# Kernel tuning notes

Measured on AMD Instinct MI355X. Metric: run time of the kernel, lower is better.

The kernel has to match this reference:

```python
import jax, jax.numpy as jnp
import numpy as np

N_NODES = 100000
N_EDGES = 3200000
IN_CH = 128
HID = 128
N_GRAPHS = 128
BN_EPS = 1e-5


def _gcn_conv(x, W, b, src, dst, n_nodes):
    # x: [N, Cin] -> [N, Cout]; PyG GCNConv: linear, add self-loops,
    # symmetric D^-1/2 A D^-1/2 normalization, scatter-add at dst, + bias.
    xw = x @ W  # [N, Cout]
    loop = jnp.arange(n_nodes, dtype=src.dtype)
    s = jnp.concatenate([src, loop])
    d = jnp.concatenate([dst, loop])
    deg = jax.ops.segment_sum(jnp.ones_like(d, dtype=xw.dtype), d, num_segments=n_nodes)
    dinv = jnp.where(deg > 0, jax.lax.rsqrt(deg), 0.0)
    coef = (dinv[s] * dinv[d])[:, None]  # [E+N, 1]
    msg = xw[s] * coef  # gather + scale
    out = jax.ops.segment_sum(msg, d, num_segments=n_nodes)  # scatter-add
    return out + b


def setup_inputs() -> dict:
    key = jax.random.key(0)
    ks = jax.random.split(key, 8)
    x = jax.random.normal(ks[0], (N_NODES, IN_CH), dtype=jnp.float32)
    edge_index = jax.random.randint(ks[1], (2, N_EDGES), 0, N_NODES, dtype=jnp.int64)
    batch = jnp.sort(jax.random.randint(ks[2], (N_NODES,), 0, N_GRAPHS, dtype=jnp.int64))
    W1 = jax.random.normal(ks[3], (IN_CH, HID), dtype=jnp.float32) / np.sqrt(IN_CH)
    W2 = jax.random.normal(ks[4], (HID, HID), dtype=jnp.float32) / np.sqrt(HID)
    fw1 = jax.random.normal(ks[5], (HID, HID // 2), dtype=jnp.float32) / np.sqrt(HID)
    cw = jax.random.normal(ks[6], (HID // 2, 2), dtype=jnp.float32) / np.sqrt(HID // 2)
    return {
        "x": x,
        "edge_index": edge_index,
        "batch": batch,
        "W1": W1,
        "b1": jnp.zeros((HID,), jnp.float32),
        "gamma": jnp.ones((HID,), jnp.float32),
        "beta": jnp.zeros((HID,), jnp.float32),
        "rmean": jnp.zeros((HID,), jnp.float32),
        "rvar": jnp.ones((HID,), jnp.float32),
        "W2": W2,
        "b2": jnp.zeros((HID,), jnp.float32),
        "fw1": fw1,
        "fb1": jnp.zeros((HID // 2,), jnp.float32),
        "cw": cw,
        "cb": jnp.zeros((2,), jnp.float32),
    }


def reference(x, edge_index, batch, W1, b1, gamma, beta, rmean, rvar, W2, b2, fw1, fb1, cw, cb):
    src, dst = edge_index[0], edge_index[1]
    h = _gcn_conv(x, W1, b1, src, dst, N_NODES)
    # BatchNorm1d in inference mode (running stats); dropout is identity in eval.
    h = (h - rmean) * jax.lax.rsqrt(rvar + BN_EPS) * gamma + beta
    h = jax.nn.relu(h)
    h = _gcn_conv(h, W2, b2, src, dst, N_NODES)
    # global_mean_pool over graphs
    sums = jax.ops.segment_sum(h, batch, num_segments=N_GRAPHS)  # [G, H]
    cnts = jax.ops.segment_sum(jnp.ones((N_NODES,), h.dtype), batch, num_segments=N_GRAPHS)
    pooled = sums / jnp.maximum(cnts, 1.0)[:, None]
    z = jax.nn.relu(pooled @ fw1 + fb1)
    return z @ cw + cb
```

## Files before the change

### kernel.cpp

```cpp
#include <hip/hip_runtime.h>
#include <hip/hip_bf16.h>

#define N_NODES 100000
#define N_EDGES 3200000
#define CH 128
#define NG 128
#define BN_EPS 1e-5f
#define NBUCK 1024
#define EPB 16384
#define NSPB 1563

using i32x4 = __attribute__((ext_vector_type(4))) int;

__device__ __forceinline__ unsigned int packq(const float* v, float inv) {
    int q0 = __float2int_rn(v[0] * inv), q1 = __float2int_rn(v[1] * inv);
    int q2 = __float2int_rn(v[2] * inv), q3 = __float2int_rn(v[3] * inv);
    return (unsigned int)(q0 & 255) | ((unsigned int)(q1 & 255) << 8) |
           ((unsigned int)(q2 & 255) << 16) | ((unsigned int)(q3 & 255) << 24);
}

__global__ __launch_bounds__(256) void k_quantx(const float* __restrict__ x,
                                                unsigned char* __restrict__ Xq,
                                                float* __restrict__ xs) {
    int t = threadIdx.x;
    int row = blockIdx.x * 16 + (t >> 4);
    int seg = t & 15;
    const float4* p = (const float4*)&x[(size_t)row * CH + seg * 8];
    float4 a = p[0], b = p[1];
    float v[8] = {a.x, a.y, a.z, a.w, b.x, b.y, b.z, b.w};
    float m = 0.f;
    #pragma unroll
    for (int i = 0; i < 8; ++i) m = fmaxf(m, fabsf(v[i]));
    m = fmaxf(m, __shfl_xor(m, 1, 64));
    m = fmaxf(m, __shfl_xor(m, 2, 64));
    m = fmaxf(m, __shfl_xor(m, 4, 64));
    m = fmaxf(m, __shfl_xor(m, 8, 64));
    float inv = (m > 0.f) ? 127.0f / m : 0.f;
    uint2 pk;
    pk.x = packq(&v[0], inv);
    pk.y = packq(&v[4], inv);
    *(uint2*)&Xq[(size_t)row * CH + seg * 8] = pk;
    if (seg == 0) xs[row] = m * (1.0f / 127.0f);
}

__global__ __launch_bounds__(256) void k_prepW(
    const float* __restrict__ W1, const float* __restrict__ W2,
    const float* __restrict__ gamma, const float* __restrict__ beta,
    const float* __restrict__ rmean, const float* __restrict__ rvar, const float* __restrict__ b1,
    unsigned char* __restrict__ Wq1T, float* __restrict__ wcs1,
    unsigned char* __restrict__ Wq2T, float* __restrict__ wcs2,
    float* __restrict__ A1, float* __restrict__ B1) {
    int t = threadIdx.x;
    const float* W = (t < 128) ? W1 : W2;
    unsigned char* WT = (t < 128) ? Wq1T : Wq2T;
    float* wcs = (t < 128) ? wcs1 : wcs2;
    int c = t & 127;
    float m = 0.f;
    for (int k = 0; k < 128; ++k) m = fmaxf(m, fabsf(W[k * CH + c]));
    float inv = (m > 0.f) ? 127.0f / m : 0.f;
    for (int k = 0; k < 128; ++k) {
        int q = __float2int_rn(W[k * CH + c] * inv);
        WT[c * CH + k] = (unsigned char)(q & 255);
    }
    wcs[c] = m * (1.0f / 127.0f);
    if (t < 128) {
        float a = gamma[c] * rsqrtf(rvar[c] + BN_EPS);
        A1[c] = a;
        B1[c] = (b1[c] - rmean[c]) * a + beta[c];
    }
}

__global__ __launch_bounds__(256) void k_bhist(const int* __restrict__ dst, int* __restrict__ bcnt) {
    __shared__ int lh[NBUCK];
    for (int i = threadIdx.x; i < NBUCK; i += 256) lh[i] = 0;
    __syncthreads();
    for (int e = blockIdx.x * 256 + threadIdx.x; e < N_EDGES; e += gridDim.x * 256)
        atomicAdd(&lh[dst[e] >> 7], 1);
    __syncthreads();
    for (int i = threadIdx.x; i < NBUCK; i += 256) {
        int v = lh[i];
        if (v) atomicAdd(&bcnt[i], v);
    }
}

__global__ __launch_bounds__(256) void k_bscan(const int* __restrict__ in, int* __restrict__ out,
                                               int* __restrict__ cur) {
    __shared__ int sm[256];
    int t = threadIdx.x;
    int4 v = *(const int4*)&in[t * 4];
    int tsum = v.x + v.y + v.z + v.w;
    sm[t] = tsum;
    __syncthreads();
    for (int off = 1; off < 256; off <<= 1) {
        int val = sm[t];
        int add = (t >= off) ? sm[t - off] : 0;
        __syncthreads();
        sm[t] = val + add;
        __syncthreads();
    }
    int excl = sm[t] - tsum;
    int o0 = excl, o1 = excl + v.x, o2 = o1 + v.y, o3 = o2 + v.z;
    out[t * 4] = o0; out[t * 4 + 1] = o1; out[t * 4 + 2] = o2; out[t * 4 + 3] = o3;
    if (cur) { cur[t * 4] = o0; cur[t * 4 + 1] = o1; cur[t * 4 + 2] = o2; cur[t * 4 + 3] = o3; }
}

__global__ __launch_bounds__(256) void k_bin(const int* __restrict__ src, const int* __restrict__ dst,
                                             int* __restrict__ bcur, unsigned int* __restrict__ pairs) {
    __shared__ int lhist[NBUCK];
    __shared__ int lbase[NBUCK];
    int t = threadIdx.x;
    for (int i = t; i < NBUCK; i += 256) lhist[i] = 0;
    __syncthreads();
    int base = blockIdx.x * EPB;
    int lim = min(base + EPB, N_EDGES);
    for (int e = base + t; e < lim; e += 256)
        atomicAdd(&lhist[dst[e] >> 7], 1);
    __syncthreads();
    for (int i = t; i < NBUCK; i += 256) {
        int h = lhist[i];
        lbase[i] = h ? atomicAdd(&bcur[i], h) : 0;
        lhist[i] = 0;
    }
    __syncthreads();
    for (int e = base + t; e < lim; e += 256) {
        int d = dst[e];
        int b = d >> 7;
        int r = atomicAdd(&lhist[b], 1);
        pairs[lbase[b] + r] = ((unsigned int)src[e] << 7) | ((unsigned int)d & 127u);
    }
}

__global__ __launch_bounds__(256) void k_bfill(const unsigned int* __restrict__ pairs,
                                               const int* __restrict__ boffs,
                                               int* __restrict__ offs, int* __restrict__ deg,
                                               float* __restrict__ dinv, int* __restrict__ perm) {
    __shared__ int lcur[1024];
    __shared__ int loff[1024];
    __shared__ int sm[256];
    int b = blockIdx.x;
    int t = threadIdx.x;
    for (int i = t; i < 1024; i += 256) lcur[i] = 0;
    __syncthreads();
    int p0 = boffs[b];
    int p1 = (b == NBUCK - 1) ? N_EDGES : boffs[b + 1];
    for (int p = p0 + t; p < p1; p += 256) {
        unsigned int e = pairs[p];
        int idx = (int)((e & 127u) << 3) | (int)((e >> 7) >> 14);
        atomicAdd(&lcur[idx], 1);
    }
    __syncthreads();
    int4 v = *(const int4*)&lcur[t * 4];
    int tsum = v.x + v.y + v.z + v.w;
    sm[t] = tsum;
    __syncthreads();
    for (int off = 1; off < 256; off <<= 1) {
        int val = sm[t];
        int add = (t >= off) ? sm[t - off] : 0;
        __syncthreads();
        sm[t] = val + add;
        __syncthreads();
    }
    int excl = sm[t] - tsum + p0;
    loff[t * 4]     = excl;
    loff[t * 4 + 1] = excl + v.x;
    loff[t * 4 + 2] = excl + v.x + v.y;
    loff[t * 4 + 3] = excl + v.x + v.y + v.z;
    lcur[t * 4] = 0; lcur[t * 4 + 1] = 0; lcur[t * 4 + 2] = 0; lcur[t * 4 + 3] = 0;
    __syncthreads();
    if (t < 128) {
        int node = (b << 7) + t;
        if (node < N_NODES) {
            int o0 = loff[t * 8];
            int o1 = (t == 127) ? p1 : loff[(t + 1) * 8];
            int cnt = o1 - o0;
            offs[node] = o0;
            deg[node] = cnt;
            dinv[node] = rsqrtf((float)(cnt + 1));
        }
    }
    __syncthreads();
    for (int p = p0 + t; p < p1; p += 256) {
        unsigned int e = pairs[p];
        int src = (int)(e >> 7);
        int idx = (int)((e & 127u) << 3) | (src >> 14);
        int r = atomicAdd(&lcur[idx], 1);
        perm[loff[idx] + r] = src;
    }
}

__global__ __launch_bounds__(256) void k_gemm_mfma(
    const unsigned char* __restrict__ Xq, const float* __restrict__ xs,
    const unsigned char* __restrict__ WT, const float* __restrict__ wcs,
    const float* __restrict__ dinvp, unsigned char* __restrict__ Yq, float* __restrict__ ospre) {
    __shared__ float ep[4][16][132];
    int t = threadIdx.x;
    int w = t >> 6;
    int lane = t & 63;
    int quad = lane >> 4, l16 = lane & 15;
    int row0 = blockIdx.x * 64 + w * 16;

    int arow = row0 + l16;
    if (arow >= N_NODES) arow = N_NODES - 1;
    i32x4 a0 = *(const i32x4*)&Xq[(size_t)arow * CH + quad * 16];
    i32x4 a1 = *(const i32x4*)&Xq[(size_t)arow * CH + 64 + quad * 16];

    i32x4 acc[8];
    #pragma unroll
    for (int i = 0; i < 8; ++i) acc[i] = (i32x4){0, 0, 0, 0};

    #pragma unroll
    for (int tt = 0; tt < 8; ++tt) {
        int n = tt * 16 + l16;
        i32x4 b0 = *(const i32x4*)&WT[(size_t)n * CH + quad * 16];
        i32x4 b1 = *(const i32x4*)&WT[(size_t)n * CH + 64 + quad * 16];
        acc[tt] = __builtin_amdgcn_mfma_i32_16x16x64_i8(a0, b0, acc[tt], 0, 0, 0);
        acc[tt] = __builtin_amdgcn_mfma_i32_16x16x64_i8(a1, b1, acc[tt], 0, 0, 0);
    }

    float xsr[4];
    #pragma unroll
    for (int r = 0; r < 4; ++r) {
        int rr = row0 + quad * 4 + r;
        xsr[r] = xs[(rr < N_NODES) ? rr : (N_NODES - 1)];
    }
    #pragma unroll
    for (int tt = 0; tt < 8; ++tt) {
        float wc = wcs[tt * 16 + l16];
        #pragma unroll
        for (int r = 0; r < 4; ++r)
            ep[w][quad * 4 + r][tt * 16 + l16] = (float)acc[tt][r] * xsr[r] * wc;
    }
    __syncthreads();

    int rl = lane >> 2, part = lane & 3;
    int grow = row0 + rl;
    float v[32];
    float m = 0.f;
    #pragma unroll
    for (int i = 0; i < 32; ++i) {
        v[i] = ep[w][rl][part * 32 + i];
        m = fmaxf(m, fabsf(v[i]));
    }
    m = fmaxf(m, __shfl_xor(m, 1, 64));
    m = fmaxf(m, __shfl_xor(m, 2, 64));
    if (grow < N_NODES) {
        float inv = (m > 0.f) ? 127.0f / m : 0.f;
        unsigned int o[8];
        #pragma unroll
        for (int q = 0; q < 8; ++q) o[q] = packq(&v[q * 4], inv);
        uint4* dst0 = (uint4*)&Yq[(size_t)grow * CH + part * 32];
        dst0[0] = make_uint4(o[0], o[1], o[2], o[3]);
        dst0[1] = make_uint4(o[4], o[5], o[6], o[7]);
        if (part == 0) ospre[grow] = (m * (1.0f / 127.0f)) * dinvp[grow];
    }
}

#define ACCI8(f, v)                                                                    \
    { int _a = (int)v.x, _b = (int)v.y;                                                \
      acc[0] += f * (float)((_a << 24) >> 24);                                         \
      acc[1] += f * (float)((_a << 16) >> 24);                                         \
      acc[2] += f * (float)((_a << 8) >> 24);                                          \
      acc[3] += f * (float)(_a >> 24);                                                 \
      acc[4] += f * (float)((_b << 24) >> 24);                                         \
      acc[5] += f * (float)((_b << 16) >> 24);                                         \
      acc[6] += f * (float)((_b << 8) >> 24);                                          \
      acc[7] += f * (float)(_b >> 24); }

#define SPMM_ROW_GATHER()                                                              \
    float di = 0.f; int beg = 0, end = 0;                                              \
    if (valid) { di = dinv[row]; beg = offs[row]; end = beg + deg[row]; }              \
    float acc[8];                                                                      \
    _Pragma("unroll") for (int j = 0; j < 8; ++j) acc[j] = 0.f;                        \
    for (int cb = beg; cb < end; cb += 8) {                                            \
        int k0 = cb + g, k1 = cb + g + 4;                                              \
        int ka0 = (k0 < end) ? k0 : (end - 1);                                         \
        int ka1 = (k1 < end) ? k1 : (end - 1);                                         \
        int s0 = perm[ka0], s1 = perm[ka1];                                            \
        float f0 = (k0 < end) ? di : 0.f;                                              \
        float f1 = (k1 < end) ? di : 0.f;                                              \
        f0 *= spre[s0]; f1 *= spre[s1];                                                \
        uint2 v0 = xq[(size_t)s0 * 16 + c];                                            \
        uint2 v1 = xq[(size_t)s1 * 16 + c];                                            \
        ACCI8(f0, v0) ACCI8(f1, v1)                                                    \
    }                                                                                  \
    _Pragma("unroll") for (int j = 0; j < 8; ++j) {                                    \
        acc[j] += __shfl_xor(acc[j], 16, 64);                                          \
        acc[j] += __shfl_xor(acc[j], 32, 64);                                          \
    }

__global__ __launch_bounds__(256) void k_spmm_bn_relu(
    const uint2* __restrict__ xq, const int* __restrict__ perm, const int* __restrict__ offs,
    const int* __restrict__ deg, const float* __restrict__ dinv, const float* __restrict__ spre,
    const float* __restrict__ A1, const float* __restrict__ B1,
    uint2* __restrict__ outq, float* __restrict__ osraw) {
    int w = threadIdx.x >> 6;
    int lane = threadIdx.x & 63;
    int g = lane >> 4, c = lane & 15;
    int base = blockIdx.x * 64;
    for (int i = 0; i < 16; ++i) {
        int row = __builtin_amdgcn_readfirstlane(base + i * 4 + w);
        bool valid = row < N_NODES;
        SPMM_ROW_GATHER()
        if (g == 0 && valid) {
            uint2 v = xq[(size_t)row * 16 + c];
            float fs = di * spre[row];
            ACCI8(fs, v)
            int ch = c * 8;
            float r[8];
            const float4* A4 = (const float4*)&A1[ch];
            const float4* B4 = (const float4*)&B1[ch];
            #pragma unroll
            for (int q = 0; q < 2; ++q) {
                float4 aa = A4[q], bb = B4[q];
                r[q * 4 + 0] = fmaxf(acc[q * 4 + 0] * aa.x + bb.x, 0.f);
                r[q * 4 + 1] = fmaxf(acc[q * 4 + 1] * aa.y + bb.y, 0.f);
                r[q * 4 + 2] = fmaxf(acc[q * 4 + 2] * aa.z + bb.z, 0.f);
                r[q * 4 + 3] = fmaxf(acc[q * 4 + 3] * aa.w + bb.w, 0.f);
            }
            float m = 0.f;
            #pragma unroll
            for (int j = 0; j < 8; ++j) m = fmaxf(m, r[j]);
            #pragma unroll
            for (int off = 1; off < 16; off <<= 1) m = fmaxf(m, __shfl_xor(m, off, 64));
            float inv = (m > 0.f) ? 127.0f / m : 0.f;
            uint2 pk;
            pk.x = packq(&r[0], inv);
            pk.y = packq(&r[4], inv);
            outq[(size_t)row * 16 + c] = pk;
            if (c == 0) osraw[row] = m * (1.0f / 127.0f);
        }
    }
}

__global__ __launch_bounds__(256) void k_spmm_pool(
    const uint2* __restrict__ xq, const int* __restrict__ perm, const int* __restrict__ offs,
    const int* __restrict__ deg, const float* __restrict__ dinv, const float* __restrict__ spre,
    const float* __restrict__ bias, const int* __restrict__ batch,
    float* __restrict__ psum, int* __restrict__ pcnt) {
    __shared__ float red[4][128];
    __shared__ int gid[4];
    int w = threadIdx.x >> 6;
    int lane = threadIdx.x & 63;
    int g = lane >> 4, c = lane & 15;
    int base = blockIdx.x * 64;
    for (int i = 0; i < 16; ++i) {
        int row = __builtin_amdgcn_readfirstlane(base + i * 4 + w);
        bool valid = row < N_NODES;
        SPMM_ROW_GATHER()
        if (g == 0) {
            int ch = c * 8;
            if (valid) {
                uint2 v = xq[(size_t)row * 16 + c];
                float fs = di * spre[row];
                ACCI8(fs, v)
                #pragma unroll
                for (int j = 0; j < 8; ++j) red[w][ch + j] = acc[j] + bias[ch + j];
            } else {
                #pragma unroll
                for (int j = 0; j < 8; ++j) red[w][ch + j] = 0.f;
            }
        }
        if (lane == 0) gid[w] = valid ? batch[row] : -1;
        __syncthreads();
        bool same = (gid[0] >= 0) && (gid[0] == gid[1]) && (gid[1] == gid[2]) && (gid[2] == gid[3]);
        int c0 = lane * 2;
        if (same) {
            if (w == 0) {
                float sx = red[0][c0] + red[1][c0] + red[2][c0] + red[3][c0];
                float sy = red[0][c0 + 1] + red[1][c0 + 1] + red[2][c0 + 1] + red[3][c0 + 1];
                unsafeAtomicAdd(&psum[gid[0] * CH + c0], sx);
                unsafeAtomicAdd(&psum[gid[0] * CH + c0 + 1], sy);
                if (lane == 0) atomicAdd(&pcnt[gid[0]], 4);
            }
        } else if (gid[w] >= 0) {
            unsafeAtomicAdd(&psum[gid[w] * CH + c0], red[w][c0]);
            unsafeAtomicAdd(&psum[gid[w] * CH + c0 + 1], red[w][c0 + 1]);
            if (lane == 0) atomicAdd(&pcnt[gid[w]], 1);
        }
        __syncthreads();
    }
}

__global__ __launch_bounds__(128) void k_head(const float* __restrict__ psum, const int* __restrict__ pcnt,
                                              const float* __restrict__ fw1, const float* __restrict__ fb1,
                                              const float* __restrict__ cw, const float* __restrict__ cb,
                                              float* __restrict__ out) {
    __shared__ float fws[128 * 64];
    for (int i = threadIdx.x; i < 128 * 64; i += 128) fws[i] = fw1[i];
    __syncthreads();
    int g = threadIdx.x;
    float z[64];
    #pragma unroll
    for (int j = 0; j < 64; ++j) z[j] = fb1[j];
    float cnt = fmaxf((float)pcnt[g], 1.f);
    float inv = 1.f / cnt;
    for (int c = 0; c < 128; ++c) {
        float p = psum[g * CH + c] * inv;
        #pragma unroll
        for (int j = 0; j < 64; ++j) z[j] += p * fws[c * 64 + j];
    }
    float o0 = cb[0], o1 = cb[1];
    #pragma unroll
    for (int j = 0; j < 64; ++j) {
        float zz = fmaxf(z[j], 0.f);
        o0 += zz * cw[j * 2];
        o1 += zz * cw[j * 2 + 1];
    }
    out[g * 2] = o0;
    out[g * 2 + 1] = o1;
}

extern "C" void kernel_launch(void* const* d_in, const int* in_sizes, int n_in,
                              void* d_out, int out_size, void* d_ws, size_t ws_size,
                              hipStream_t stream) {
    const float* x     = (const float*)d_in[0];
    const int*   ei    = (const int*)d_in[1];
    const int*   batch = (const int*)d_in[2];
    const float* W1    = (const float*)d_in[3];
    const float* b1    = (const float*)d_in[4];
    const float* gamma = (const float*)d_in[5];
    const float* beta  = (const float*)d_in[6];
    const float* rmean = (const float*)d_in[7];
    const float* rvar  = (const float*)d_in[8];
    const float* W2    = (const float*)d_in[9];
    const float* b2    = (const float*)d_in[10];
    const float* fw1   = (const float*)d_in[11];
    const float* fb1   = (const float*)d_in[12];
    const float* cw    = (const float*)d_in[13];
    const float* cb    = (const float*)d_in[14];
    const int* srcp = ei;
    const int* dstp = ei + N_EDGES;

    char* w = (char*)d_ws;
    int*   bcnt  = (int*)w;   w += 4096;
    float* psum  = (float*)w; w += 65536;
    int*   pcnt  = (int*)w;   w += 512;
    size_t zbytes = 4096 + 65536 + 512;
    int*   deg   = (int*)w;   w += 400000;
    int*   offs  = (int*)w;   w += 400000;
    float* dinv  = (float*)w; w += 400000;
    float* xsA   = (float*)w; w += 400000;
    float* spreA = (float*)w; w += 400000;
    float* srawB = (float*)w; w += 400000;
    float* spreC = (float*)w; w += 400000;
    float* A1    = (float*)w; w += 512;
    float* B1    = (float*)w; w += 512;
    float* wcs1  = (float*)w; w += 512;
    float* wcs2  = (float*)w; w += 512;
    unsigned char* Wq1T = (unsigned char*)w; w += 16384;
    unsigned char* Wq2T = (unsigned char*)w; w += 16384;
    int*   boffs = (int*)w;   w += 4096;
    int*   bcur  = (int*)w;   w += 4096;
    unsigned int* pairs = (unsigned int*)w; w += 12800000;
    int*   perm  = (int*)w;   w += 12800000;
    unsigned char* Xq   = (unsigned char*)w; w += 12800000;
    unsigned char* bufA = (unsigned char*)w; w += 12800000;
    unsigned char* bufB = (unsigned char*)w; w += 12800000;
    unsigned char* bufC = (unsigned char*)w; w += 12800000;

    hipMemsetAsync(d_ws, 0, zbytes, stream);
    k_quantx<<<6250, 256, 0, stream>>>(x, Xq, xsA);
    k_bhist<<<200, 256, 0, stream>>>(dstp, bcnt);
    k_bscan<<<1, 256, 0, stream>>>(bcnt, boffs, bcur);
    k_bin<<<(N_EDGES + EPB - 1) / EPB, 256, 0, stream>>>(srcp, dstp, bcur, pairs);
    k_bfill<<<NBUCK, 256, 0, stream>>>(pairs, boffs, offs, deg, dinv, perm);
    k_prepW<<<1, 256, 0, stream>>>(W1, W2, gamma, beta, rmean, rvar, b1,
                                   Wq1T, wcs1, Wq2T, wcs2, A1, B1);
    k_gemm_mfma<<<1563, 256, 0, stream>>>(Xq, xsA, Wq1T, wcs1, dinv, bufA, spreA);
    k_spmm_bn_relu<<<NSPB, 256, 0, stream>>>((const uint2*)bufA, perm, offs, deg, dinv, spreA,
                                             A1, B1, (uint2*)bufB, srawB);
    k_gemm_mfma<<<1563, 256, 0, stream>>>(bufB, srawB, Wq2T, wcs2, dinv, bufC, spreC);
    k_spmm_pool<<<NSPB, 256, 0, stream>>>((const uint2*)bufC, perm, offs, deg, dinv, spreC,
                                          b2, batch, psum, pcnt);
    k_head<<<1, 128, 0, stream>>>(psum, pcnt, fw1, fb1, cw, cb, (float*)d_out);
}
```

Measured before the change: 555.3 us.

## Fuse input quantization into first GEMM and interleave two rows per SpMM wave

Drops the separate quantize-x kernel. The first GEMM now reads fp32 x directly, computes a per-row scale and packs int8 in registers before the MFMA, which saves a write and re-read of the quantized matrix and one launch. The SpMM kernels now gather two destination rows at once per wave, using 4 edges per step per row instead of 8 for one row. This gives more independent loads in flight, but lanes sit idle when the two rows have different degrees. The epilogues move into helper functions.

```diff
diff --git a/kernel.cpp b/kernel.cpp
--- a/kernel.cpp
+++ b/kernel.cpp
@@ -17,30 +17,6 @@
     int q2 = __float2int_rn(v[2] * inv), q3 = __float2int_rn(v[3] * inv);
     return (unsigned int)(q0 & 255) | ((unsigned int)(q1 & 255) << 8) |
            ((unsigned int)(q2 & 255) << 16) | ((unsigned int)(q3 & 255) << 24);
-}
-
-__global__ __launch_bounds__(256) void k_quantx(const float* __restrict__ x,
-                                                unsigned char* __restrict__ Xq,
-                                                float* __restrict__ xs) {
-    int t = threadIdx.x;
-    int row = blockIdx.x * 16 + (t >> 4);
-    int seg = t & 15;
-    const float4* p = (const float4*)&x[(size_t)row * CH + seg * 8];
-    float4 a = p[0], b = p[1];
-    float v[8] = {a.x, a.y, a.z, a.w, b.x, b.y, b.z, b.w};
-    float m = 0.f;
-    #pragma unroll
-    for (int i = 0; i < 8; ++i) m = fmaxf(m, fabsf(v[i]));
-    m = fmaxf(m, __shfl_xor(m, 1, 64));
-    m = fmaxf(m, __shfl_xor(m, 2, 64));
-    m = fmaxf(m, __shfl_xor(m, 4, 64));
-    m = fmaxf(m, __shfl_xor(m, 8, 64));
-    float inv = (m > 0.f) ? 127.0f / m : 0.f;
-    uint2 pk;
-    pk.x = packq(&v[0], inv);
-    pk.y = packq(&v[4], inv);
-    *(uint2*)&Xq[(size_t)row * CH + seg * 8] = pk;
-    if (seg == 0) xs[row] = m * (1.0f / 127.0f);
 }
 
 __global__ __launch_bounds__(256) void k_prepW(
@@ -188,6 +164,96 @@
     }
 }
 
+__global__ __launch_bounds__(256) void k_gemm_f32(
+    const float* __restrict__ X,
+    const unsigned char* __restrict__ WT, const float* __restrict__ wcs,
+    const float* __restrict__ dinvp, unsigned char* __restrict__ Yq, float* __restrict__ ospre) {
+    __shared__ float ep[4][16][132];
+    int t = threadIdx.x;
+    int w = t >> 6;
+    int lane = t & 63;
+    int quad = lane >> 4, l16 = lane & 15;
+    int row0 = blockIdx.x * 64 + w * 16;
+
+    int arow = row0 + l16;
+    if (arow >= N_NODES) arow = N_NODES - 1;
+
+    float xv[32];
+    {
+        const float4* p0 = (const float4*)&X[(size_t)arow * CH + quad * 16];
+        const float4* p1 = (const float4*)&X[(size_t)arow * CH + 64 + quad * 16];
+        #pragma unroll
+        for (int q = 0; q < 4; ++q) {
+            float4 f = p0[q];
+            xv[q * 4 + 0] = f.x; xv[q * 4 + 1] = f.y; xv[q * 4 + 2] = f.z; xv[q * 4 + 3] = f.w;
+        }
+        #pragma unroll
+        for (int q = 0; q < 4; ++q) {
+            float4 f = p1[q];
+            xv[16 + q * 4 + 0] = f.x; xv[16 + q * 4 + 1] = f.y;
+            xv[16 + q * 4 + 2] = f.z; xv[16 + q * 4 + 3] = f.w;
+        }
+    }
+    float m = 0.f;
+    #pragma unroll
+    for (int j = 0; j < 32; ++j) m = fmaxf(m, fabsf(xv[j]));
+    m = fmaxf(m, __shfl_xor(m, 16, 64));
+    m = fmaxf(m, __shfl_xor(m, 32, 64));
+    float inv = (m > 0.f) ? 127.0f / m : 0.f;
+    float ms = m * (1.0f / 127.0f);
+    unsigned int pk[8];
+    #pragma unroll
+    for (int j = 0; j < 8; ++j) pk[j] = packq(&xv[j * 4], inv);
+    i32x4 a0 = (i32x4){(int)pk[0], (int)pk[1], (int)pk[2], (int)pk[3]};
+    i32x4 a1 = (i32x4){(int)pk[4], (int)pk[5], (int)pk[6], (int)pk[7]};
+
+    i32x4 acc[8];
+    #pragma unroll
+    for (int i = 0; i < 8; ++i) acc[i] = (i32x4){0, 0, 0, 0};
+    #pragma unroll
+    for (int tt = 0; tt < 8; ++tt) {
+        int n = tt * 16 + l16;
+        i32x4 b0 = *(const i32x4*)&WT[(size_t)n * CH + quad * 16];
+        i32x4 b1 = *(const i32x4*)&WT[(size_t)n * CH + 64 + quad * 16];
+        acc[tt] = __builtin_amdgcn_mfma_i32_16x16x64_i8(a0, b0, acc[tt], 0, 0, 0);
+        acc[tt] = __builtin_amdgcn_mfma_i32_16x16x64_i8(a1, b1, acc[tt], 0, 0, 0);
+    }
+
+    float xsr[4];
+    #pragma unroll
+    for (int r = 0; r < 4; ++r) xsr[r] = __shfl(ms, quad * 4 + r, 64);
+    #pragma unroll
+    for (int tt = 0; tt < 8; ++tt) {
+        float wc = wcs[tt * 16 + l16];
+        #pragma unroll
+        for (int r = 0; r < 4; ++r)
+            ep[w][quad * 4 + r][tt * 16 + l16] = (float)acc[tt][r] * xsr[r] * wc;
+    }
+    __syncthreads();
+
+    int rl = lane >> 2, part = lane & 3;
+    int grow = row0 + rl;
+    float v[32];
+    float mm = 0.f;
+    #pragma unroll
+    for (int i = 0; i < 32; ++i) {
+        v[i] = ep[w][rl][part * 32 + i];
+        mm = fmaxf(mm, fabsf(v[i]));
+    }
+    mm = fmaxf(mm, __shfl_xor(mm, 1, 64));
+    mm = fmaxf(mm, __shfl_xor(mm, 2, 64));
+    if (grow < N_NODES) {
+        float inv2 = (mm > 0.f) ? 127.0f / mm : 0.f;
+        unsigned int o[8];
+        #pragma unroll
+        for (int q = 0; q < 8; ++q) o[q] = packq(&v[q * 4], inv2);
+        uint4* dst0 = (uint4*)&Yq[(size_t)grow * CH + part * 32];
+        dst0[0] = make_uint4(o[0], o[1], o[2], o[3]);
+        dst0[1] = make_uint4(o[4], o[5], o[6], o[7]);
+        if (part == 0) ospre[grow] = (mm * (1.0f / 127.0f)) * dinvp[grow];
+    }
+}
+
 __global__ __launch_bounds__(256) void k_gemm_mfma(
     const unsigned char* __restrict__ Xq, const float* __restrict__ xs,
     const unsigned char* __restrict__ WT, const float* __restrict__ wcs,
@@ -255,7 +321,7 @@
     }
 }
 
-#define ACCI8(f, v)                                                                    \
+#define ACCI8P(acc, f, v)                                                              \
     { int _a = (int)v.x, _b = (int)v.y;                                                \
       acc[0] += f * (float)((_a << 24) >> 24);                                         \
       acc[1] += f * (float)((_a << 16) >> 24);                                         \
@@ -266,27 +332,107 @@
       acc[6] += f * (float)((_b << 8) >> 24);                                          \
       acc[7] += f * (float)(_b >> 24); }
 
-#define SPMM_ROW_GATHER()                                                              \
-    float di = 0.f; int beg = 0, end = 0;                                              \
-    if (valid) { di = dinv[row]; beg = offs[row]; end = beg + deg[row]; }              \
-    float acc[8];                                                                      \
-    _Pragma("unroll") for (int j = 0; j < 8; ++j) acc[j] = 0.f;                        \
-    for (int cb = beg; cb < end; cb += 8) {                                            \
-        int k0 = cb + g, k1 = cb + g + 4;                                              \
-        int ka0 = (k0 < end) ? k0 : (end - 1);                                         \
-        int ka1 = (k1 < end) ? k1 : (end - 1);                                         \
-        int s0 = perm[ka0], s1 = perm[ka1];                                            \
-        float f0 = (k0 < end) ? di : 0.f;                                              \
-        float f1 = (k1 < end) ? di : 0.f;                                              \
-        f0 *= spre[s0]; f1 *= spre[s1];                                                \
-        uint2 v0 = xq[(size_t)s0 * 16 + c];                                            \
-        uint2 v1 = xq[(size_t)s1 * 16 + c];                                            \
-        ACCI8(f0, v0) ACCI8(f1, v1)                                                    \
+#define SPMM_PAIR_GATHER(ii)                                                           \
+    int rowA = __builtin_amdgcn_readfirstlane(base + (ii) * 4 + w);                    \
+    int rowB = __builtin_amdgcn_readfirstlane(base + (ii) * 4 + 4 + w);                \
+    bool valA = rowA < N_NODES, valB = rowB < N_NODES;                                 \
+    float diA = 0.f, diB = 0.f;                                                        \
+    int begA = 0, endA = 0, begB = 0, endB = 0;                                        \
+    if (valA) { diA = dinv[rowA]; begA = offs[rowA]; endA = begA + deg[rowA]; }        \
+    if (valB) { diB = dinv[rowB]; begB = offs[rowB]; endB = begB + deg[rowB]; }        \
+    float accA[8], accB[8];                                                            \
+    _Pragma("unroll") for (int j = 0; j < 8; ++j) { accA[j] = 0.f; accB[j] = 0.f; }    \
+    int cbA = begA, cbB = begB;                                                        \
+    while (cbA < endA || cbB < endB) {                                                 \
+        int kA = cbA + g, kB = cbB + g;                                                \
+        int kaA = (kA < endA) ? kA : ((endA > 1) ? endA - 1 : 0);                      \
+        int kaB = (kB < endB) ? kB : ((endB > 1) ? endB - 1 : 0);                      \
+        int sA = perm[kaA], sB = perm[kaB];                                            \
+        float fA = (kA < endA) ? diA : 0.f;                                            \
+        float fB = (kB < endB) ? diB : 0.f;                                            \
+        fA *= spre[sA]; fB *= spre[sB];                                                \
+        uint2 vA = xq[(size_t)sA * 16 + c];                                            \
+        uint2 vB = xq[(size_t)sB * 16 + c];                                            \
+        ACCI8P(accA, fA, vA) ACCI8P(accB, fB, vB)                                      \
+        cbA += 4; cbB += 4;                                                            \
     }                                                                                  \
     _Pragma("unroll") for (int j = 0; j < 8; ++j) {                                    \
-        acc[j] += __shfl_xor(acc[j], 16, 64);                                          \
-        acc[j] += __shfl_xor(acc[j], 32, 64);                                          \
-    }
+        accA[j] += __shfl_xor(accA[j], 16, 64);                                        \
+        accA[j] += __shfl_xor(accA[j], 32, 64);                                        \
+        accB[j] += __shfl_xor(accB[j], 16, 64);                                        \
+        accB[j] += __shfl_xor(accB[j], 32, 64);                                        \
+    }
+
+__device__ __forceinline__ void bn_epi(int row, float di, float* acc, int c,
+                                       const uint2* __restrict__ xq, const float* __restrict__ spre,
+                                       const float* __restrict__ A1, const float* __restrict__ B1,
+                                       uint2* __restrict__ outq, float* __restrict__ osraw) {
+    uint2 v = xq[(size_t)row * 16 + c];
+    float fs = di * spre[row];
+    ACCI8P(acc, fs, v)
+    int ch = c * 8;
+    float r[8];
+    const float4* A4 = (const float4*)&A1[ch];
+    const float4* B4 = (const float4*)&B1[ch];
+    #pragma unroll
+    for (int q = 0; q < 2; ++q) {
+        float4 aa = A4[q], bb = B4[q];
+        r[q * 4 + 0] = fmaxf(acc[q * 4 + 0] * aa.x + bb.x, 0.f);
+        r[q * 4 + 1] = fmaxf(acc[q * 4 + 1] * aa.y + bb.y, 0.f);
+        r[q * 4 + 2] = fmaxf(acc[q * 4 + 2] * aa.z + bb.z, 0.f);
+        r[q * 4 + 3] = fmaxf(acc[q * 4 + 3] * aa.w + bb.w, 0.f);
+    }
+    float m = 0.f;
+    #pragma unroll
+    for (int i = 0; i < 8; ++i) m = fmaxf(m, r[i]);
+    #pragma unroll
+    for (int off = 1; off < 16; off <<= 1) m = fmaxf(m, __shfl_xor(m, off, 64));
+    float inv = (m > 0.f) ? 127.0f / m : 0.f;
+    uint2 pk;
+    pk.x = packq(&r[0], inv);
+    pk.y = packq(&r[4], inv);
+    outq[(size_t)row * 16 + c] = pk;
+    if (c == 0) osraw[row] = m * (1.0f / 127.0f);
+}
+
+__device__ __forceinline__ void pool_epi(int row, bool valid, float di, float* acc,
+                                         int w, int lane, int g, int c,
+                                         const uint2* __restrict__ xq, const float* __restrict__ spre,
+                                         const float* __restrict__ bias, const int* __restrict__ batch,
+                                         float* __restrict__ psum, int* __restrict__ pcnt,
+                                         float (*red)[128], int* gid) {
+    if (g == 0) {
+        int ch = c * 8;
+        if (valid) {
+            uint2 v = xq[(size_t)row * 16 + c];
+            float fs = di * spre[row];
+            ACCI8P(acc, fs, v)
+            #pragma unroll
+            for (int j = 0; j < 8; ++j) red[w][ch + j] = acc[j] + bias[ch + j];
+        } else {
+            #pragma unroll
+            for (int j = 0; j < 8; ++j) red[w][ch + j] = 0.f;
+        }
+    }
+    if (lane == 0) gid[w] = valid ? batch[row] : -1;
+    __syncthreads();
+    bool same = (gid[0] >= 0) && (gid[0] == gid[1]) && (gid[1] == gid[2]) && (gid[2] == gid[3]);
+    int c0 = lane * 2;
+    if (same) {
+        if (w == 0) {
+            float sx = red[0][c0] + red[1][c0] + red[2][c0] + red[3][c0];
+            float sy = red[0][c0 + 1] + red[1][c0 + 1] + red[2][c0 + 1] + red[3][c0 + 1];
+            unsafeAtomicAdd(&psum[gid[0] * CH + c0], sx);
+            unsafeAtomicAdd(&psum[gid[0] * CH + c0 + 1], sy);
+            if (lane == 0) atomicAdd(&pcnt[gid[0]], 4);
+        }
+    } else if (gid[w] >= 0) {
+        unsafeAtomicAdd(&psum[gid[w] * CH + c0], red[w][c0]);
+        unsafeAtomicAdd(&psum[gid[w] * CH + c0 + 1], red[w][c0 + 1]);
+        if (lane == 0) atomicAdd(&pcnt[gid[w]], 1);
+    }
+    __syncthreads();
+}
 
 __global__ __launch_bounds__(256) void k_spmm_bn_relu(
     const uint2* __restrict__ xq, const int* __restrict__ perm, const int* __restrict__ offs,
@@ -297,38 +443,10 @@
     int lane = threadIdx.x & 63;
     int g = lane >> 4, c = lane & 15;
     int base = blockIdx.x * 64;
-    for (int i = 0; i < 16; ++i) {
-        int row = __builtin_amdgcn_readfirstlane(base + i * 4 + w);
-        bool valid = row < N_NODES;
-        SPMM_ROW_GATHER()
-        if (g == 0 && valid) {
-            uint2 v = xq[(size_t)row * 16 + c];
-            float fs = di * spre[row];
-            ACCI8(fs, v)
-            int ch = c * 8;
-            float r[8];
-            const float4* A4 = (const float4*)&A1[ch];
-            const float4* B4 = (const float4*)&B1[ch];
-            #pragma unroll
-            for (int q = 0; q < 2; ++q) {
-                float4 aa = A4[q], bb = B4[q];
-                r[q * 4 + 0] = fmaxf(acc[q * 4 + 0] * aa.x + bb.x, 0.f);
-                r[q * 4 + 1] = fmaxf(acc[q * 4 + 1] * aa.y + bb.y, 0.f);
-                r[q * 4 + 2] = fmaxf(acc[q * 4 + 2] * aa.z + bb.z, 0.f);
-                r[q * 4 + 3] = fmaxf(acc[q * 4 + 3] * aa.w + bb.w, 0.f);
-            }
-            float m = 0.f;
-            #pragma unroll
-            for (int j = 0; j < 8; ++j) m = fmaxf(m, r[j]);
-            #pragma unroll
-            for (int off = 1; off < 16; off <<= 1) m = fmaxf(m, __shfl_xor(m, off, 64));
-            float inv = (m > 0.f) ? 127.0f / m : 0.f;
-            uint2 pk;
-            pk.x = packq(&r[0], inv);
-            pk.y = packq(&r[4], inv);
-            outq[(size_t)row * 16 + c] = pk;
-            if (c == 0) osraw[row] = m * (1.0f / 127.0f);
-        }
+    for (int i = 0; i < 16; i += 2) {
+        SPMM_PAIR_GATHER(i)
+        if (g == 0 && valA) bn_epi(rowA, diA, accA, c, xq, spre, A1, B1, outq, osraw);
+        if (g == 0 && valB) bn_epi(rowB, diB, accB, c, xq, spre, A1, B1, outq, osraw);
     }
 }
 
@@ -343,41 +461,10 @@
     int lane = threadIdx.x & 63;
     int g = lane >> 4, c = lane & 15;
     int base = blockIdx.x * 64;
-    for (int i = 0; i < 16; ++i) {
-        int row = __builtin_amdgcn_readfirstlane(base + i * 4 + w);
-        bool valid = row < N_NODES;
-        SPMM_ROW_GATHER()
-        if (g == 0) {
-            int ch = c * 8;
-            if (valid) {
-                uint2 v = xq[(size_t)row * 16 + c];
-                float fs = di * spre[row];
-                ACCI8(fs, v)
-                #pragma unroll
-                for (int j = 0; j < 8; ++j) red[w][ch + j] = acc[j] + bias[ch + j];
-            } else {
-                #pragma unroll
-                for (int j = 0; j < 8; ++j) red[w][ch + j] = 0.f;
-            }
-        }
-        if (lane == 0) gid[w] = valid ? batch[row] : -1;
-        __syncthreads();
-        bool same = (gid[0] >= 0) && (gid[0] == gid[1]) && (gid[1] == gid[2]) && (gid[2] == gid[3]);
-        int c0 = lane * 2;
-        if (same) {
-            if (w == 0) {
-                float sx = red[0][c0] + red[1][c0] + red[2][c0] + red[3][c0];
-                float sy = red[0][c0 + 1] + red[1][c0 + 1] + red[2][c0 + 1] + red[3][c0 + 1];
-                unsafeAtomicAdd(&psum[gid[0] * CH + c0], sx);
-                unsafeAtomicAdd(&psum[gid[0] * CH + c0 + 1], sy);
-                if (lane == 0) atomicAdd(&pcnt[gid[0]], 4);
-            }
-        } else if (gid[w] >= 0) {
-            unsafeAtomicAdd(&psum[gid[w] * CH + c0], red[w][c0]);
-            unsafeAtomicAdd(&psum[gid[w] * CH + c0 + 1], red[w][c0 + 1]);
-            if (lane == 0) atomicAdd(&pcnt[gid[w]], 1);
-        }
-        __syncthreads();
+    for (int i = 0; i < 16; i += 2) {
+        SPMM_PAIR_GATHER(i)
+        pool_epi(rowA, valA, diA, accA, w, lane, g, c, xq, spre, bias, batch, psum, pcnt, red, gid);
+        pool_epi(rowB, valB, diB, accB, w, lane, g, c, xq, spre, bias, batch, psum, pcnt, red, gid);
     }
 }
 
@@ -439,7 +526,6 @@
     int*   deg   = (int*)w;   w += 400000;
     int*   offs  = (int*)w;   w += 400000;
     float* dinv  = (float*)w; w += 400000;
-    float* xsA   = (float*)w; w += 400000;
     float* spreA = (float*)w; w += 400000;
     float* srawB = (float*)w; w += 400000;
     float* spreC = (float*)w; w += 400000;
@@ -453,20 +539,18 @@
     int*   bcur  = (int*)w;   w += 4096;
     unsigned int* pairs = (unsigned int*)w; w += 12800000;
     int*   perm  = (int*)w;   w += 12800000;
-    unsigned char* Xq   = (unsigned char*)w; w += 12800000;
     unsigned char* bufA = (unsigned char*)w; w += 12800000;
     unsigned char* bufB = (unsigned char*)w; w += 12800000;
     unsigned char* bufC = (unsigned char*)w; w += 12800000;
 
     hipMemsetAsync(d_ws, 0, zbytes, stream);
-    k_quantx<<<6250, 256, 0, stream>>>(x, Xq, xsA);
     k_bhist<<<200, 256, 0, stream>>>(dstp, bcnt);
     k_bscan<<<1, 256, 0, stream>>>(bcnt, boffs, bcur);
     k_bin<<<(N_EDGES + EPB - 1) / EPB, 256, 0, stream>>>(srcp, dstp, bcur, pairs);
     k_bfill<<<NBUCK, 256, 0, stream>>>(pairs, boffs, offs, deg, dinv, perm);
     k_prepW<<<1, 256, 0, stream>>>(W1, W2, gamma, beta, rmean, rvar, b1,
                                    Wq1T, wcs1, Wq2T, wcs2, A1, B1);
-    k_gemm_mfma<<<1563, 256, 0, stream>>>(Xq, xsA, Wq1T, wcs1, dinv, bufA, spreA);
+    k_gemm_f32<<<1563, 256, 0, stream>>>(x, Wq1T, wcs1, dinv, bufA, spreA);
     k_spmm_bn_relu<<<NSPB, 256, 0, stream>>>((const uint2*)bufA, perm, offs, deg, dinv, spreA,
                                              A1, B1, (uint2*)bufB, srawB);
     k_gemm_mfma<<<1563, 256, 0, stream>>>(bufB, srawB, Wq2T, wcs2, dinv, bufC, spreC);
```

Result: faster. 518.2 us (-6.7%).

## Fuse input quantization into GEMM and second GEMM into first SpMM

Applied to the files above, without the earlier changes.

Removes the standalone x quantization kernel by quantizing fp32 rows to int8 inside the first MFMA GEMM, with the per-row scale computed via cross-lane shuffles. Also fuses the layer-2 GEMM into the first SpMM+BN+ReLU kernel: quantized rows are staged in LDS, multiplied with W2 via int8 MFMA, requantized and written out. This drops two launches and two intermediate global buffers (Xq, bufB) and their round trips, at the cost of more LDS use and extra syncs in the SpMM kernel.

```diff
diff --git a/kernel.cpp b/kernel.cpp
--- a/kernel.cpp
+++ b/kernel.cpp
@@ -17,30 +17,6 @@
     int q2 = __float2int_rn(v[2] * inv), q3 = __float2int_rn(v[3] * inv);
     return (unsigned int)(q0 & 255) | ((unsigned int)(q1 & 255) << 8) |
            ((unsigned int)(q2 & 255) << 16) | ((unsigned int)(q3 & 255) << 24);
-}
-
-__global__ __launch_bounds__(256) void k_quantx(const float* __restrict__ x,
-                                                unsigned char* __restrict__ Xq,
-                                                float* __restrict__ xs) {
-    int t = threadIdx.x;
-    int row = blockIdx.x * 16 + (t >> 4);
-    int seg = t & 15;
-    const float4* p = (const float4*)&x[(size_t)row * CH + seg * 8];
-    float4 a = p[0], b = p[1];
-    float v[8] = {a.x, a.y, a.z, a.w, b.x, b.y, b.z, b.w};
-    float m = 0.f;
-    #pragma unroll
-    for (int i = 0; i < 8; ++i) m = fmaxf(m, fabsf(v[i]));
-    m = fmaxf(m, __shfl_xor(m, 1, 64));
-    m = fmaxf(m, __shfl_xor(m, 2, 64));
-    m = fmaxf(m, __shfl_xor(m, 4, 64));
-    m = fmaxf(m, __shfl_xor(m, 8, 64));
-    float inv = (m > 0.f) ? 127.0f / m : 0.f;
-    uint2 pk;
-    pk.x = packq(&v[0], inv);
-    pk.y = packq(&v[4], inv);
-    *(uint2*)&Xq[(size_t)row * CH + seg * 8] = pk;
-    if (seg == 0) xs[row] = m * (1.0f / 127.0f);
 }
 
 __global__ __launch_bounds__(256) void k_prepW(
@@ -188,8 +164,8 @@
     }
 }
 
-__global__ __launch_bounds__(256) void k_gemm_mfma(
-    const unsigned char* __restrict__ Xq, const float* __restrict__ xs,
+__global__ __launch_bounds__(256) void k_gemm_f32(
+    const float* __restrict__ X,
     const unsigned char* __restrict__ WT, const float* __restrict__ wcs,
     const float* __restrict__ dinvp, unsigned char* __restrict__ Yq, float* __restrict__ ospre) {
     __shared__ float ep[4][16][132];
@@ -201,13 +177,39 @@
 
     int arow = row0 + l16;
     if (arow >= N_NODES) arow = N_NODES - 1;
-    i32x4 a0 = *(const i32x4*)&Xq[(size_t)arow * CH + quad * 16];
-    i32x4 a1 = *(const i32x4*)&Xq[(size_t)arow * CH + 64 + quad * 16];
+
+    float xv[32];
+    {
+        const float4* p0 = (const float4*)&X[(size_t)arow * CH + quad * 16];
+        const float4* p1 = (const float4*)&X[(size_t)arow * CH + 64 + quad * 16];
+        #pragma unroll
+        for (int q = 0; q < 4; ++q) {
+            float4 f = p0[q];
+            xv[q * 4 + 0] = f.x; xv[q * 4 + 1] = f.y; xv[q * 4 + 2] = f.z; xv[q * 4 + 3] = f.w;
+        }
+        #pragma unroll
+        for (int q = 0; q < 4; ++q) {
+            float4 f = p1[q];
+            xv[16 + q * 4 + 0] = f.x; xv[16 + q * 4 + 1] = f.y;
+            xv[16 + q * 4 + 2] = f.z; xv[16 + q * 4 + 3] = f.w;
+        }
+    }
+    float m = 0.f;
+    #pragma unroll
+    for (int j = 0; j < 32; ++j) m = fmaxf(m, fabsf(xv[j]));
+    m = fmaxf(m, __shfl_xor(m, 16, 64));
+    m = fmaxf(m, __shfl_xor(m, 32, 64));
+    float inv = (m > 0.f) ? 127.0f / m : 0.f;
+    float ms = m * (1.0f / 127.0f);
+    unsigned int pk[8];
+    #pragma unroll
+    for (int j = 0; j < 8; ++j) pk[j] = packq(&xv[j * 4], inv);
+    i32x4 a0 = (i32x4){(int)pk[0], (int)pk[1], (int)pk[2], (int)pk[3]};
+    i32x4 a1 = (i32x4){(int)pk[4], (int)pk[5], (int)pk[6], (int)pk[7]};
 
     i32x4 acc[8];
     #pragma unroll
     for (int i = 0; i < 8; ++i) acc[i] = (i32x4){0, 0, 0, 0};
-
     #pragma unroll
     for (int tt = 0; tt < 8; ++tt) {
         int n = tt * 16 + l16;
@@ -219,10 +221,7 @@
 
     float xsr[4];
     #pragma unroll
-    for (int r = 0; r < 4; ++r) {
-        int rr = row0 + quad * 4 + r;
-        xsr[r] = xs[(rr < N_NODES) ? rr : (N_NODES - 1)];
-    }
+    for (int r = 0; r < 4; ++r) xsr[r] = __shfl(ms, quad * 4 + r, 64);
     #pragma unroll
     for (int tt = 0; tt < 8; ++tt) {
         float wc = wcs[tt * 16 + l16];
@@ -235,23 +234,23 @@
     int rl = lane >> 2, part = lane & 3;
     int grow = row0 + rl;
     float v[32];
-    float m = 0.f;
+    float mm = 0.f;
     #pragma unroll
     for (int i = 0; i < 32; ++i) {
         v[i] = ep[w][rl][part * 32 + i];
-        m = fmaxf(m, fabsf(v[i]));
-    }
-    m = fmaxf(m, __shfl_xor(m, 1, 64));
-    m = fmaxf(m, __shfl_xor(m, 2, 64));
+        mm = fmaxf(mm, fabsf(v[i]));
+    }
+    mm = fmaxf(mm, __shfl_xor(mm, 1, 64));
+    mm = fmaxf(mm, __shfl_xor(mm, 2, 64));
     if (grow < N_NODES) {
-        float inv = (m > 0.f) ? 127.0f / m : 0.f;
+        float inv2 = (mm > 0.f) ? 127.0f / mm : 0.f;
         unsigned int o[8];
         #pragma unroll
-        for (int q = 0; q < 8; ++q) o[q] = packq(&v[q * 4], inv);
+        for (int q = 0; q < 8; ++q) o[q] = packq(&v[q * 4], inv2);
         uint4* dst0 = (uint4*)&Yq[(size_t)grow * CH + part * 32];
         dst0[0] = make_uint4(o[0], o[1], o[2], o[3]);
         dst0[1] = make_uint4(o[4], o[5], o[6], o[7]);
-        if (part == 0) ospre[grow] = (m * (1.0f / 127.0f)) * dinvp[grow];
+        if (part == 0) ospre[grow] = (mm * (1.0f / 127.0f)) * dinvp[grow];
     }
 }
 
@@ -288,47 +287,121 @@
         acc[j] += __shfl_xor(acc[j], 32, 64);                                          \
     }
 
-__global__ __launch_bounds__(256) void k_spmm_bn_relu(
+__global__ __launch_bounds__(256) void k_spmm_fused1(
     const uint2* __restrict__ xq, const int* __restrict__ perm, const int* __restrict__ offs,
     const int* __restrict__ deg, const float* __restrict__ dinv, const float* __restrict__ spre,
     const float* __restrict__ A1, const float* __restrict__ B1,
-    uint2* __restrict__ outq, float* __restrict__ osraw) {
+    const unsigned char* __restrict__ WT, const float* __restrict__ wcs,
+    unsigned char* __restrict__ Yq, float* __restrict__ ospre) {
+    __shared__ unsigned char rows8[64][128];
+    __shared__ float sraw[64];
     int w = threadIdx.x >> 6;
     int lane = threadIdx.x & 63;
     int g = lane >> 4, c = lane & 15;
     int base = blockIdx.x * 64;
+
     for (int i = 0; i < 16; ++i) {
         int row = __builtin_amdgcn_readfirstlane(base + i * 4 + w);
         bool valid = row < N_NODES;
         SPMM_ROW_GATHER()
-        if (g == 0 && valid) {
-            uint2 v = xq[(size_t)row * 16 + c];
-            float fs = di * spre[row];
-            ACCI8(fs, v)
-            int ch = c * 8;
-            float r[8];
-            const float4* A4 = (const float4*)&A1[ch];
-            const float4* B4 = (const float4*)&B1[ch];
-            #pragma unroll
-            for (int q = 0; q < 2; ++q) {
-                float4 aa = A4[q], bb = B4[q];
-                r[q * 4 + 0] = fmaxf(acc[q * 4 + 0] * aa.x + bb.x, 0.f);
-                r[q * 4 + 1] = fmaxf(acc[q * 4 + 1] * aa.y + bb.y, 0.f);
-                r[q * 4 + 2] = fmaxf(acc[q * 4 + 2] * aa.z + bb.z, 0.f);
-                r[q * 4 + 3] = fmaxf(acc[q * 4 + 3] * aa.w + bb.w, 0.f);
+        if (g == 0) {
+            int rl = i * 4 + w;
+            if (valid) {
+                uint2 v = xq[(size_t)row * 16 + c];
+                float fs = di * spre[row];
+                ACCI8(fs, v)
+                int ch = c * 8;
+                float r[8];
+                const float4* A4 = (const float4*)&A1[ch];
+                const float4* B4 = (const float4*)&B1[ch];
+                #pragma unroll
+                for (int q = 0; q < 2; ++q) {
+                    float4 aa = A4[q], bb = B4[q];
+                    r[q * 4 + 0] = fmaxf(acc[q * 4 + 0] * aa.x + bb.x, 0.f);
+                    r[q * 4 + 1] = fmaxf(acc[q * 4 + 1] * aa.y + bb.y, 0.f);
+                    r[q * 4 + 2] = fmaxf(acc[q * 4 + 2] * aa.z + bb.z, 0.f);
+                    r[q * 4 + 3] = fmaxf(acc[q * 4 + 3] * aa.w + bb.w, 0.f);
+                }
+                float m = 0.f;
+                #pragma unroll
+                for (int j = 0; j < 8; ++j) m = fmaxf(m, r[j]);
+                #pragma unroll
+                for (int off = 1; off < 16; off <<= 1) m = fmaxf(m, __shfl_xor(m, off, 64));
+                float inv = (m > 0.f) ? 127.0f / m : 0.f;
+                uint2 pk;
+                pk.x = packq(&r[0], inv);
+                pk.y = packq(&r[4], inv);
+                *(uint2*)&rows8[rl][c * 8] = pk;
+                if (c == 0) sraw[rl] = m * (1.0f / 127.0f);
+            } else {
+                *(uint2*)&rows8[rl][c * 8] = make_uint2(0u, 0u);
+                if (c == 0) sraw[rl] = 0.f;
             }
-            float m = 0.f;
-            #pragma unroll
-            for (int j = 0; j < 8; ++j) m = fmaxf(m, r[j]);
-            #pragma unroll
-            for (int off = 1; off < 16; off <<= 1) m = fmaxf(m, __shfl_xor(m, off, 64));
-            float inv = (m > 0.f) ? 127.0f / m : 0.f;
-            uint2 pk;
-            pk.x = packq(&r[0], inv);
-            pk.y = packq(&r[4], inv);
-            outq[(size_t)row * 16 + c] = pk;
-            if (c == 0) osraw[row] = m * (1.0f / 127.0f);
-        }
+        }
+    }
+    __syncthreads();
+
+    i32x4 a0 = *(const i32x4*)&rows8[w * 16 + c][g * 16];
+    i32x4 a1 = *(const i32x4*)&rows8[w * 16 + c][64 + g * 16];
+    i32x4 acc2[8];
+    #pragma unroll
+    for (int i = 0; i < 8; ++i) acc2[i] = (i32x4){0, 0, 0, 0};
+    #pragma unroll
+    for (int tt = 0; tt < 8; ++tt) {
+        int n = tt * 16 + c;
+        i32x4 b0 = *(const i32x4*)&WT[(size_t)n * CH + g * 16];
+        i32x4 b1 = *(const i32x4*)&WT[(size_t)n * CH + 64 + g * 16];
+        acc2[tt] = __builtin_amdgcn_mfma_i32_16x16x64_i8(a0, b0, acc2[tt], 0, 0, 0);
+        acc2[tt] = __builtin_amdgcn_mfma_i32_16x16x64_i8(a1, b1, acc2[tt], 0, 0, 0);
+    }
+    float xsr[4];
+    #pragma unroll
+    for (int r = 0; r < 4; ++r) xsr[r] = sraw[w * 16 + g * 4 + r];
+    float mr[4] = {0.f, 0.f, 0.f, 0.f};
+    #pragma unroll
+    for (int tt = 0; tt < 8; ++tt) {
+        float wc = wcs[tt * 16 + c];
+        #pragma unroll
+        for (int r = 0; r < 4; ++r)
+            mr[r] = fmaxf(mr[r], fabsf((float)acc2[tt][r] * xsr[r] * wc));
+    }
+    #pragma unroll
+    for (int r = 0; r < 4; ++r) {
+        mr[r] = fmaxf(mr[r], __shfl_xor(mr[r], 1, 64));
+        mr[r] = fmaxf(mr[r], __shfl_xor(mr[r], 2, 64));
+        mr[r] = fmaxf(mr[r], __shfl_xor(mr[r], 4, 64));
+        mr[r] = fmaxf(mr[r], __shfl_xor(mr[r], 8, 64));
+    }
+    float qs[4];
+    #pragma unroll
+    for (int r = 0; r < 4; ++r) qs[r] = (mr[r] > 0.f) ? 127.0f / mr[r] : 0.f;
+    __syncthreads();
+    #pragma unroll
+    for (int tt = 0; tt < 8; ++tt) {
+        float wc = wcs[tt * 16 + c];
+        #pragma unroll
+        for (int r = 0; r < 4; ++r) {
+            int q = __float2int_rn((float)acc2[tt][r] * xsr[r] * wc * qs[r]);
+            rows8[w * 16 + g * 4 + r][tt * 16 + c] = (unsigned char)(q & 255);
+        }
+    }
+    if (c == 0) {
+        #pragma unroll
+        for (int r = 0; r < 4; ++r) {
+            int grow = base + w * 16 + g * 4 + r;
+            if (grow < N_NODES) ospre[grow] = (mr[r] * (1.0f / 127.0f)) * dinv[grow];
+        }
+    }
+    __syncthreads();
+    const uint4* rs = (const uint4*)rows8;
+    int t = threadIdx.x;
+    #pragma unroll
+    for (int j = 0; j < 2; ++j) {
+        int idx = t + j * 256;
+        int rl = idx >> 3;
+        int grow = base + rl;
+        if (grow < N_NODES)
+            ((uint4*)Yq)[(size_t)grow * 8 + (idx & 7)] = rs[idx];
     }
 }
 
@@ -439,9 +512,7 @@
     int*   deg   = (int*)w;   w += 400000;
     int*   offs  = (int*)w;   w += 400000;
     float* dinv  = (float*)w; w += 400000;
-    float* xsA   = (float*)w; w += 400000;
     float* spreA = (float*)w; w += 400000;
-    float* srawB = (float*)w; w += 400000;
     float* spreC = (float*)w; w += 400000;
     float* A1    = (float*)w; w += 512;
     float* B1    = (float*)w; w += 512;
@@ -453,23 +524,19 @@
     int*   bcur  = (int*)w;   w += 4096;
     unsigned int* pairs = (unsigned int*)w; w += 12800000;
     int*   perm  = (int*)w;   w += 12800000;
-    unsigned char* Xq   = (unsigned char*)w; w += 12800000;
     unsigned char* bufA = (unsigned char*)w; w += 12800000;
-    unsigned char* bufB = (unsigned char*)w; w += 12800000;
     unsigned char* bufC = (unsigned char*)w; w += 12800000;
 
     hipMemsetAsync(d_ws, 0, zbytes, stream);
-    k_quantx<<<6250, 256, 0, stream>>>(x, Xq, xsA);
     k_bhist<<<200, 256, 0, stream>>>(dstp, bcnt);
     k_bscan<<<1, 256, 0, stream>>>(bcnt, boffs, bcur);
     k_bin<<<(N_EDGES + EPB - 1) / EPB, 256, 0, stream>>>(srcp, dstp, bcur, pairs);
     k_bfill<<<NBUCK, 256, 0, stream>>>(pairs, boffs, offs, deg, dinv, perm);
     k_prepW<<<1, 256, 0, stream>>>(W1, W2, gamma, beta, rmean, rvar, b1,
                                    Wq1T, wcs1, Wq2T, wcs2, A1, B1);
-    k_gemm_mfma<<<1563, 256, 0, stream>>>(Xq, xsA, Wq1T, wcs1, dinv, bufA, spreA);
-    k_spmm_bn_relu<<<NSPB, 256, 0, stream>>>((const uint2*)bufA, perm, offs, deg, dinv, spreA,
-                                             A1, B1, (uint2*)bufB, srawB);
-    k_gemm_mfma<<<1563, 256, 0, stream>>>(bufB, srawB, Wq2T, wcs2, dinv, bufC, spreC);
+    k_gemm_f32<<<1563, 256, 0, stream>>>(x, Wq1T, wcs1, dinv, bufA, spreA);
+    k_spmm_fused1<<<NSPB, 256, 0, stream>>>((const uint2*)bufA, perm, offs, deg, dinv, spreA,
+                                            A1, B1, Wq2T, wcs2, bufC, spreC);
     k_spmm_pool<<<NSPB, 256, 0, stream>>>((const uint2*)bufC, perm, offs, deg, dinv, spreC,
                                           b2, batch, psum, pcnt);
     k_head<<<1, 128, 0, stream>>>(psum, pcnt, fw1, fb1, cw, cb, (float*)d_out);
```

Result: slower. 581.8 us (+4.8%).
